# Performance work log

Measured on AMD Instinct MI355X. Metric: run time of the kernel, lower is better.

Reference implementation:

```python
import jax, jax.numpy as jnp
import numpy as np


def setup_inputs() -> dict:
    key = jax.random.key(0)
    k1, k2 = jax.random.split(key)
    B, C, H, W = 4, 128, 256, 448
    feat1 = jax.random.normal(k1, (B, C, H, W), dtype=jnp.float32)
    feat2 = jax.random.normal(k2, (B, C, H, W), dtype=jnp.float32)
    return {"feat1": feat1, "feat2": feat2, "max_disp": 4}


def reference(feat1, feat2, max_disp):
    # PWC-Net cost volume: kernel_size=1, stride1=stride2=1.
    # cost[b, s, h, w] = mean_c feat1[b,c,h,w] * feat2_pad[b,c,h+i,w+j]
    # where s enumerates (i, j) in [0, 2*max_disp]^2, row-major (matching
    # the torch nested i/j loop + cat order).
    B, C, H, W = feat1.shape
    md = int(max_disp)
    num_shifts = 2 * md + 1
    feat2_pad = jnp.pad(feat2, ((0, 0), (0, 0), (md, md), (md, md)))

    ij = jnp.arange(num_shifts)
    offsets = jnp.stack(jnp.meshgrid(ij, ij, indexing="ij"), axis=-1).reshape(-1, 2)  # (S*S, 2)

    def one_shift(off):
        sl = jax.lax.dynamic_slice(feat2_pad, (0, 0, off[0], off[1]), (B, C, H, W))
        return jnp.mean(feat1 * sl, axis=1)  # (B, H, W)

    cost = jax.vmap(one_shift)(offsets)        # (81, B, H, W)
    return jnp.transpose(cost, (1, 0, 2, 3))   # (B, 81, H, W)
```

## Files before the change

kernel.cpp:

```cpp
#include <hip/hip_runtime.h>


typedef __attribute__((ext_vector_type(4))) float f32x4;

#define GLAS(p) ((const __attribute__((address_space(1))) unsigned int*)(p))
#define LDAS(p) ((__attribute__((address_space(3))) unsigned int*)(p))

__global__ __launch_bounds__(1024, 4) void cv_kernel(
    const float* __restrict__ feat1,
    const float* __restrict__ feat2,
    const float* __restrict__ zws,
    float* __restrict__ out)
{
    constexpr int C = 128, H = 256, W = 448;
    constexpr size_t HW = (size_t)H * W;
    constexpr int ROWB = 114 * 16;
    constexpr int BUFB = 10 * ROWB;
    __shared__ __align__(16) char f2s[3 * BUFB];

    const int tid  = threadIdx.x;
    const int wid  = tid >> 6;
    const int lane = tid & 63;

    const int lin = (blockIdx.x & 7) * 128 + (blockIdx.x >> 3);
    const int b = lin >> 8, h = lin & 255;

    const int it = (tid < 1008) ? tid : 1007;
    const int di = it / 112;
    const int G  = it - di * 112;

    for (int i = tid; i < (int)sizeof(f2s) / 16; i += 1024)
        *(f32x4*)(f2s + i * 16) = (f32x4){0.f, 0.f, 0.f, 0.f};

    const int nIss = (wid < 4) ? 2 : 1;
    const float* sp[2]; unsigned sstep[2]; int sdst[2];
#pragma unroll
    for (int k = 0; k < 2; ++k) {
        if (k < nIss) {
            const int j  = wid + 16 * k;
            const int r  = j >> 1, hf = j & 1;
            const int colf = hf * 224 + ((lane < 56) ? lane * 4 : 220);
            if (r == 9) {
                sp[k] = feat1 + ((size_t)b * C * H + (size_t)h) * W + colf;
                sstep[k] = (unsigned)HW;
            } else {
                const int hr = h + r - 4;
                const bool ok = (hr >= 0) && (hr < H);
                sp[k] = ok ? (feat2 + ((size_t)b * C * H + (size_t)hr) * W + colf) : zws;
                sstep[k] = ok ? (unsigned)HW : 0u;
            }
            sdst[k] = r * ROWB + 16 + hf * 896;
        }
    }

    const int r2o = di * ROWB + G * 16;
    const int r1o = 9 * ROWB + (G + 1) * 16;

    float acc[9][4];
#pragma unroll
    for (int j = 0; j < 9; ++j)
#pragma unroll
        for (int p = 0; p < 4; ++p) acc[j][p] = 0.0f;

    __syncthreads();

#define STAGE(BUFOFS) do { \
    _Pragma("unroll") \
    for (int k = 0; k < 2; ++k) { \
        if (k < nIss) { \
            if (lane < 56) \
                __builtin_amdgcn_global_load_lds(GLAS(sp[k]), \
                    LDAS(f2s + (BUFOFS) + sdst[k]), 16, 0, 0); \
            sp[k] += sstep[k]; \
        } \
    } } while (0)

#define BODY(BUF, NBUF, MODE) do { \
    if ((MODE) <= 1) { \
        if (wid < 4) asm volatile("s_waitcnt vmcnt(2)" ::: "memory"); \
        else         asm volatile("s_waitcnt vmcnt(1)" ::: "memory"); \
    } else { \
        asm volatile("s_waitcnt vmcnt(0)" ::: "memory"); \
    } \
    __builtin_amdgcn_s_barrier(); \
    __builtin_amdgcn_sched_barrier(0); \
    if ((MODE) == 0) STAGE((NBUF) * BUFB); \
    { \
        const char* lb = f2s + (BUF) * BUFB; \
        const f32x4 L  = *(const f32x4*)(lb + r2o); \
        const f32x4 Cq = *(const f32x4*)(lb + r2o + 16); \
        const f32x4 R  = *(const f32x4*)(lb + r2o + 32); \
        const f32x4 A  = *(const f32x4*)(lb + r1o); \
        const float w[12] = {L.x, L.y, L.z, L.w, Cq.x, Cq.y, Cq.z, Cq.w, \
                             R.x, R.y, R.z, R.w}; \
        const float a[4] = {A.x, A.y, A.z, A.w}; \
        _Pragma("unroll") \
        for (int dj = 0; dj < 9; ++dj) { \
            _Pragma("unroll") \
            for (int p = 0; p < 4; ++p) \
                acc[dj][p] = fmaf(a[p], w[dj + p], acc[dj][p]); \
        } \
    } } while (0)

    STAGE(0 * BUFB);
    STAGE(1 * BUFB);

#pragma unroll 1
    for (int g = 0; g < 42; ++g) {
        BODY(0, 2, 0);
        BODY(1, 0, 0);
        BODY(2, 1, 0);
    }
    BODY(0, 2, 1);
    BODY(1, 0, 2);

#undef STAGE
#undef BODY

    if (tid < 1008) {
        const float s = 1.0f / 128.0f;
        float* ob = out + (((size_t)(b * 81 + di * 9)) * H + h) * W + G * 4;
#pragma unroll
        for (int dj = 0; dj < 9; ++dj) {
            f32x4 ov = {acc[dj][0] * s, acc[dj][1] * s,
                        acc[dj][2] * s, acc[dj][3] * s};
            *(f32x4*)(ob + (size_t)dj * HW) = ov;
        }
    }
}

extern "C" void kernel_launch(void* const* d_in, const int* in_sizes, int n_in,
                              void* d_out, int out_size, void* d_ws, size_t ws_size,
                              hipStream_t stream) {
    const float* feat1 = (const float*)d_in[0];
    const float* feat2 = (const float*)d_in[1];
    float* out = (float*)d_out;
    hipMemsetAsync(d_ws, 0, 256, stream);
    cv_kernel<<<dim3(1024), dim3(1024), 0, stream>>>(
        feat1, feat2, (const float*)d_ws, out);
}
```

Measured before the change: 277.8 us.

## Load feat1 directly into registers with prefetch instead of staging through LDS

Each thread now reads its own feat1 vector straight from global memory into registers, one channel ahead, instead of having waves copy the feat1 row into shared memory. This shrinks each LDS buffer from 10 rows to 9 and cuts the async LDS-issuing waves. It also removes one LDS read per iteration. The pipeline prologue now issues two feat2 stages up front, and the loop rotation is adjusted so the vmcnt waits still cover both the register loads and the LDS loads. The trade-off is more per-thread global loads with small 16-byte accesses, plus extra registers for the prefetch.

```diff
diff --git a/kernel.cpp b/kernel.cpp
--- a/kernel.cpp
+++ b/kernel.cpp
@@ -15,7 +15,7 @@
     constexpr int C = 128, H = 256, W = 448;
     constexpr size_t HW = (size_t)H * W;
     constexpr int ROWB = 114 * 16;
-    constexpr int BUFB = 10 * ROWB;
+    constexpr int BUFB = 9 * ROWB;
     __shared__ __align__(16) char f2s[3 * BUFB];
 
     const int tid  = threadIdx.x;
@@ -32,7 +32,7 @@
     for (int i = tid; i < (int)sizeof(f2s) / 16; i += 1024)
         *(f32x4*)(f2s + i * 16) = (f32x4){0.f, 0.f, 0.f, 0.f};
 
-    const int nIss = (wid < 4) ? 2 : 1;
+    const int nIss = (wid < 2) ? 2 : 1;
     const float* sp[2]; unsigned sstep[2]; int sdst[2];
 #pragma unroll
     for (int k = 0; k < 2; ++k) {
@@ -40,21 +40,16 @@
             const int j  = wid + 16 * k;
             const int r  = j >> 1, hf = j & 1;
             const int colf = hf * 224 + ((lane < 56) ? lane * 4 : 220);
-            if (r == 9) {
-                sp[k] = feat1 + ((size_t)b * C * H + (size_t)h) * W + colf;
-                sstep[k] = (unsigned)HW;
-            } else {
-                const int hr = h + r - 4;
-                const bool ok = (hr >= 0) && (hr < H);
-                sp[k] = ok ? (feat2 + ((size_t)b * C * H + (size_t)hr) * W + colf) : zws;
-                sstep[k] = ok ? (unsigned)HW : 0u;
-            }
+            const int hr = h + r - 4;
+            const bool ok = (hr >= 0) && (hr < H);
+            sp[k] = ok ? (feat2 + ((size_t)b * C * H + (size_t)hr) * W + colf) : zws;
+            sstep[k] = ok ? (unsigned)HW : 0u;
             sdst[k] = r * ROWB + 16 + hf * 896;
         }
     }
 
     const int r2o = di * ROWB + G * 16;
-    const int r1o = 9 * ROWB + (G + 1) * 16;
+    unsigned f1o = (unsigned)(((b * C * H) + h) * W + G * 4);
 
     float acc[9][4];
 #pragma unroll
@@ -75,46 +70,70 @@
         } \
     } } while (0)
 
+#define COMP(BUFOFS) do { \
+    const char* lb = f2s + (BUFOFS); \
+    const f32x4 L  = *(const f32x4*)(lb + r2o); \
+    const f32x4 Cq = *(const f32x4*)(lb + r2o + 16); \
+    const f32x4 R  = *(const f32x4*)(lb + r2o + 32); \
+    const float w[12] = {L.x, L.y, L.z, L.w, Cq.x, Cq.y, Cq.z, Cq.w, \
+                         R.x, R.y, R.z, R.w}; \
+    const float a[4] = {f1cur.x, f1cur.y, f1cur.z, f1cur.w}; \
+    _Pragma("unroll") \
+    for (int dj = 0; dj < 9; ++dj) { \
+        _Pragma("unroll") \
+        for (int p = 0; p < 4; ++p) \
+            acc[dj][p] = fmaf(a[p], w[dj + p], acc[dj][p]); \
+    } } while (0)
+
 #define BODY(BUF, NBUF, MODE) do { \
     if ((MODE) <= 1) { \
-        if (wid < 4) asm volatile("s_waitcnt vmcnt(2)" ::: "memory"); \
+        if (wid < 2) asm volatile("s_waitcnt vmcnt(2)" ::: "memory"); \
         else         asm volatile("s_waitcnt vmcnt(1)" ::: "memory"); \
     } else { \
         asm volatile("s_waitcnt vmcnt(0)" ::: "memory"); \
     } \
     __builtin_amdgcn_s_barrier(); \
     __builtin_amdgcn_sched_barrier(0); \
+    f32x4 f1next; \
+    if ((MODE) <= 1) { \
+        f1next = *(const f32x4*)(feat1 + f1o); f1o += (unsigned)HW; \
+        __builtin_amdgcn_sched_barrier(0); \
+    } \
     if ((MODE) == 0) STAGE((NBUF) * BUFB); \
-    { \
-        const char* lb = f2s + (BUF) * BUFB; \
-        const f32x4 L  = *(const f32x4*)(lb + r2o); \
-        const f32x4 Cq = *(const f32x4*)(lb + r2o + 16); \
-        const f32x4 R  = *(const f32x4*)(lb + r2o + 32); \
-        const f32x4 A  = *(const f32x4*)(lb + r1o); \
-        const float w[12] = {L.x, L.y, L.z, L.w, Cq.x, Cq.y, Cq.z, Cq.w, \
-                             R.x, R.y, R.z, R.w}; \
-        const float a[4] = {A.x, A.y, A.z, A.w}; \
-        _Pragma("unroll") \
-        for (int dj = 0; dj < 9; ++dj) { \
-            _Pragma("unroll") \
-            for (int p = 0; p < 4; ++p) \
-                acc[dj][p] = fmaf(a[p], w[dj + p], acc[dj][p]); \
-        } \
-    } } while (0)
+    __builtin_amdgcn_sched_barrier(0); \
+    COMP((BUF) * BUFB); \
+    if ((MODE) <= 1) f1cur = f1next; \
+  } while (0)
 
     STAGE(0 * BUFB);
-    STAGE(1 * BUFB);
+    f32x4 f1cur = *(const f32x4*)(feat1 + f1o); f1o += (unsigned)HW;
+
+    {
+        asm volatile("s_waitcnt vmcnt(0)" ::: "memory");
+        __builtin_amdgcn_s_barrier();
+        __builtin_amdgcn_sched_barrier(0);
+        f32x4 f1next = *(const f32x4*)(feat1 + f1o); f1o += (unsigned)HW;
+        __builtin_amdgcn_sched_barrier(0);
+        STAGE(1 * BUFB);
+        STAGE(2 * BUFB);
+        __builtin_amdgcn_sched_barrier(0);
+        COMP(0 * BUFB);
+        f1cur = f1next;
+    }
 
 #pragma unroll 1
-    for (int g = 0; g < 42; ++g) {
-        BODY(0, 2, 0);
+    for (int g = 0; g < 41; ++g) {
         BODY(1, 0, 0);
         BODY(2, 1, 0);
+        BODY(0, 2, 0);
     }
+    BODY(1, 0, 0);
+    BODY(2, 1, 0);
     BODY(0, 2, 1);
     BODY(1, 0, 2);
 
 #undef STAGE
+#undef COMP
 #undef BODY
 
     if (tid < 1008) {
```

Measured after the change: 442.8 us. 59.4% more time.
